# Kernel optimization log

Measured on AMD Instinct MI355X. Metric: run time of the kernel, lower is better.

The kernel has to match this reference:

```python
import jax, jax.numpy as jnp
import numpy as np

B, C, H, W = 8, 256, 96, 96
NQ, NCLS = 100, 12
OBJ_CH = NCLS - 2 + 1  # 11
EPS = 1e-6


def conv2d(x, w, b, pad):
    out = jax.lax.conv_general_dilated(x, w, (1, 1), [(pad, pad), (pad, pad)],
                                       dimension_numbers=('NCHW', 'OIHW', 'NCHW'))
    return out + b[None, :, None, None]


def conv1d(x, w, b):
    out = jax.lax.conv_general_dilated(x, w, (1,), [(0, 0)],
                                       dimension_numbers=('NCH', 'OIH', 'NCH'))
    return out + b[None, :, None]


def adaptive_avg_pool_1d(x, out_size):
    # x: [..., L]; torch AdaptiveAvgPool semantics: bin i = mean(x[floor(i*L/o):ceil((i+1)*L/o)])
    L = x.shape[-1]
    i = np.arange(out_size)
    starts = (i * L) // out_size
    ends = -((-(i + 1) * L) // out_size)
    csum = jnp.concatenate([jnp.zeros(x.shape[:-1] + (1,), x.dtype), jnp.cumsum(x, -1)], -1)
    sizes = jnp.asarray((ends - starts).astype(np.float32))
    return (csum[..., ends] - csum[..., starts]) / sizes


def local_max(p):
    # 8-neighbor local maximum with zero padding, thresholded at EPS
    pd = jnp.pad(p, ((0, 0), (0, 0), (1, 1), (1, 1)))
    m = ((p >= pd[:, :, :-2, 1:-1]) & (p >= pd[:, :, 2:, 1:-1]) &
         (p >= pd[:, :, 1:-1, :-2]) & (p >= pd[:, :, 1:-1, 2:]) &
         (p >= pd[:, :, :-2, :-2]) & (p >= pd[:, :, :-2, 2:]) &
         (p >= pd[:, :, 2:, :-2]) & (p >= pd[:, :, 2:, 2:]) & (p >= EPS))
    return m.astype(p.dtype)


def mask_and_nms(probs):
    # one-hot mask from argmax over foreground channels, then add local-max map
    oh = jax.nn.one_hot(jnp.argmax(probs[:, :-1], axis=1), probs.shape[1], axis=1, dtype=probs.dtype)
    p = probs * oh
    return p + local_max(p)


def head(x, w1, b1, w2, b2):
    return conv2d(jax.nn.relu(conv2d(x, w1, b1, 1)), w2, b2, 0)


def setup_inputs() -> dict:
    key = jax.random.key(0)
    ks = jax.random.split(key, 20)
    rn = lambda k, s: jax.random.normal(k, s, jnp.float32) * 0.02
    z = lambda n: jnp.zeros((n,), jnp.float32)
    return {
        'x': jax.random.normal(ks[0], (B, C, H, W), jnp.float32),
        'y': jax.random.normal(ks[1], (B, C, H, W), jnp.float32),
        'pos_embeddings': jax.random.normal(ks[2], (1, C, H, W), jnp.float32),
        'lw1': rn(ks[3], (C, C, 3, 3)), 'lb1': z(C),
        'lw2': rn(ks[4], (2, C, 1, 1)), 'lb2': z(2),
        'rw1': rn(ks[5], (C, C, 3, 3)), 'rb1': z(C),
        'rw2': rn(ks[6], (2, C, 1, 1)), 'rb2': z(2),
        'ow1': rn(ks[7], (C, C, 3, 3)), 'ob1': z(C),
        'ow2': rn(ks[8], (OBJ_CH, C, 1, 1)), 'ob2': z(OBJ_CH),
        'cw1': rn(ks[9], (64, C, 3, 3)), 'cb1': z(64),
        'cw2': rn(ks[10], (32, 64, 3, 3)), 'cb2': z(32),
        'cm_lw': rn(ks[11], (778 * 2, 778 * 32)), 'cm_lb': z(778 * 2),
        'c1d_w': rn(ks[12], (C, 2, 3)), 'c1d_b': z(C),
        'q_lw': rn(ks[13], (NQ * C, C)), 'q_lb': z(NQ * C),
    }


def reference(x, y, pos_embeddings, lw1, lb1, lw2, lb2, rw1, rb1, rw2, rb2,
              ow1, ob1, ow2, ob2, cw1, cb1, cw2, cb2, cm_lw, cm_lb,
              c1d_w, c1d_b, q_lw, q_lb):
    b = x.shape[0]
    left_logits = head(x, lw1, lb1, lw2, lb2)
    right_logits = head(x, rw1, rb1, rw2, rb2)
    obj_logits = head(x, ow1, ob1, ow2, ob2)

    left_p = mask_and_nms(jax.nn.softmax(left_logits, axis=1))
    right_p = mask_and_nms(jax.nn.softmax(right_logits, axis=1))
    obj_p = mask_and_nms(jax.nn.softmax(obj_logits, axis=1))

    hw = H * W
    idx_l = jax.lax.top_k(left_p[:, 0].reshape(b, hw), 40)[1]
    idx_r = jax.lax.top_k(right_p[:, 0].reshape(b, hw), 40)[1]
    idx_o = jax.lax.top_k(obj_p[:, :-1].reshape(b, OBJ_CH - 1, hw).max(axis=1), 20)[1]
    idx = jnp.concatenate([idx_l, idx_r, idx_o], axis=1)  # [B, 100]

    xf = x.reshape(b, C, hw)
    topk_proposals = jnp.take_along_axis(xf, jnp.broadcast_to(idx[:, None, :], (b, C, NQ)), axis=2)
    pf = jnp.broadcast_to(pos_embeddings, (b, C, H, W)).reshape(b, C, hw)
    topk_pos = jnp.take_along_axis(pf, jnp.broadcast_to(idx[:, None, :], (b, C, NQ)), axis=2)

    # contact map estimation branch
    h = jax.nn.relu(conv2d(y, cw1, cb1, 1))
    h = jax.nn.relu(conv2d(h, cw2, cb2, 1))  # [B,32,H,W]
    h = jnp.mean(h, axis=3)                  # adaptive pool width -> 1
    h = adaptive_avg_pool_1d(h, 778)         # [B,32,778]
    cm = h.reshape(b, -1) @ cm_lw.T + cm_lb  # [B,1556]
    contact_map = cm.reshape(b, 2, 778, 1)

    # ContactMapConvolution
    cc = conv1d(contact_map.reshape(b, 2, 778), c1d_w, c1d_b)  # [B,C,776]
    cc = jnp.mean(cc, axis=2)                                  # [B,C]
    feat = (cc @ q_lw.T + q_lb).reshape(b, C, NQ)              # [B,C,100]

    topk_proposals = topk_proposals + feat
    return (topk_proposals, topk_pos, left_logits, right_logits, obj_logits, contact_map)
```

## Files before the change

kernel.cpp:

```cpp
#include <hip/hip_runtime.h>
#include <float.h>
#include <math.h>

#define B_ 8
#define C_ 256
#define H_ 96
#define W_ 96
#define HW_ 9216
#define NQ_ 100
#define EPS_ 1e-6f
#define PADW_ 98
#define PADIMG_ 9604
#define PALLOC_ 76880

typedef unsigned short ushort_t;
typedef __attribute__((ext_vector_type(8))) short bf16x8;
typedef __attribute__((ext_vector_type(16))) float f32x16;

typedef __attribute__((address_space(3))) unsigned int as3_u32;
typedef __attribute__((address_space(1))) unsigned int as1_u32;

__device__ __forceinline__ void gl16(const void* g, void* l) {
    __builtin_amdgcn_global_load_lds(
        (const as1_u32*)(unsigned long long)g,
        (as3_u32*)(unsigned int)(unsigned long long)l, 16, 0, 0);
}

__device__ __forceinline__ ushort_t bf16_of(float v) {
    unsigned u = __float_as_uint(v);
    u += 0x7fffu + ((u >> 16) & 1u);
    return (ushort_t)(u >> 16);
}
__device__ __forceinline__ float f_of_bf16(ushort_t h) {
    return __uint_as_float((unsigned)h << 16);
}

__global__ __launch_bounds__(256)
void zero_border_kernel(ushort_t* __restrict__ bh, ushort_t* __restrict__ bl, int Cch)
{
    int per = 388 * Cch / 8;
    int id = blockIdx.x * 256 + threadIdx.x;
    if (id >= 8 * per) return;
    int b = id / per, i = id - b * per;
    int pi = (i * 8) / Cch, c8 = (i * 8) % Cch;
    int yy, xx;
    if (pi < 98)      { yy = 0;            xx = pi; }
    else if (pi < 196){ yy = 97;           xx = pi - 98; }
    else if (pi < 292){ yy = pi - 195;     xx = 0; }
    else              { yy = pi - 291;     xx = 97; }
    size_t base = ((size_t)b * PADIMG_ + yy * PADW_ + xx) * Cch + c8;
    *(bf16x8*)&bh[base] = (bf16x8)(short)0;
    *(bf16x8*)&bl[base] = (bf16x8)(short)0;
}

__global__ __launch_bounds__(256)
void tsplit_kernel(const float* __restrict__ in, ushort_t* __restrict__ oh,
                   ushort_t* __restrict__ ol, int Cch)
{
    __shared__ float T[32][33];
    const int tx = threadIdx.x & 31, ty = threadIdx.x >> 5;
    const int p0 = blockIdx.x * 32, ci0 = blockIdx.y * 32, b = blockIdx.z;
#pragma unroll
    for (int i = 0; i < 4; ++i)
        T[ty + 8*i][tx] = in[((size_t)b*Cch + ci0 + ty + 8*i)*HW_ + p0 + tx];
    __syncthreads();
    const int y = p0 / 96, x0 = p0 - y * 96;
    const size_t Pp = (size_t)b*PADIMG_ + (size_t)(y + 1)*PADW_ + x0 + 1;
#pragma unroll
    for (int i = 0; i < 4; ++i) {
        float v = T[tx][ty + 8*i];
        ushort_t hi = bf16_of(v);
        float lo = v - f_of_bf16(hi);
        size_t o = (Pp + ty + 8*i)*Cch + ci0 + tx;
        oh[o] = hi;
        ol[o] = bf16_of(lo);
    }
}

__global__ __launch_bounds__(256)
void repack_kernel(const float* __restrict__ w, ushort_t* __restrict__ wh,
                   ushort_t* __restrict__ wl, int Cout, int Cin)
{
    int id = blockIdx.x*256 + threadIdx.x;
    int tot = 9*Cout*Cin;
    if (id >= tot) return;
    int tap = id / (Cout*Cin);
    int r   = id - tap*(Cout*Cin);
    int g   = r / (Cout*16);
    int r2  = r - g*(Cout*16);
    int oc  = r2 >> 4, cr = r2 & 15;
    int ci  = g*16 + cr;
    float v = w[((size_t)oc*Cin + ci)*9 + tap];
    ushort_t hi = bf16_of(v);
    wh[id] = hi;
    wl[id] = bf16_of(v - f_of_bf16(hi));
}

__global__ __launch_bounds__(256)
void pack_heads3_kernel(const float* lb1, const float* rb1, const float* ob1,
                        const float* lw2, const float* rw2, const float* ow2,
                        const float* lb2, const float* rb2, const float* ob2,
                        float* __restrict__ bias1all, float* __restrict__ w2all,
                        float* __restrict__ b2all)
{
    int i = blockIdx.x * 256 + threadIdx.x;
    if (i < 768) bias1all[i] = (i < 256) ? lb1[i] : (i < 512) ? rb1[i-256] : ob1[i-512];
    if (i < 33) {
        int h = i / 11, k = i - h*11;
        b2all[i] = (h == 0) ? (k < 2 ? lb2[k] : 0.f)
                 : (h == 1) ? (k < 2 ? rb2[k] : 0.f)
                 : ob2[k];
    }
    if (i < 3*11*256) {
        int h = i / 2816, r = i - h*2816;
        int k = r / 256, oc = r - k*256;
        float v = 0.f;
        if (h == 0)      { if (k < 2) v = lw2[k*256 + oc]; }
        else if (h == 1) { if (k < 2) v = rw2[k*256 + oc]; }
        else             v = ow2[k*256 + oc];
        w2all[i] = v;
    }
}

template<int WM, int WN, int MFR, int NFR, int CIN, int MODE>
__global__ __launch_bounds__(WM*WN*64, (WM*WN + 3) / 4)
void conv_gemm_kernel(const ushort_t* __restrict__ Agh, const ushort_t* __restrict__ Agl,
                      const ushort_t* __restrict__ Wgh, const ushort_t* __restrict__ Wgl,
                      const float* __restrict__ bias1,
                      ushort_t* __restrict__ Oth, ushort_t* __restrict__ Otl,
                      float* __restrict__ outf)
{
    constexpr int NW    = WM*WN;
    constexpr int NT    = NW*64;
    constexpr int BM    = WM*MFR*32;
    constexpr int COUT  = WN*NFR*32;
    constexpr int NG    = CIN/16;
    constexpr int APAD  = 512;
    constexpr int ASZ   = 2*APAD*16;
    constexpr int AROUNDS = 32;
    static_assert(BM == 288, "BM must be 288");

    __shared__ __align__(16) ushort_t ALds[2*ASZ];

    const int tid  = threadIdx.x;
    const int lane = tid & 63;
    const int wid  = __builtin_amdgcn_readfirstlane(tid >> 6);
    const int wm   = wid / WN, wn = wid % WN;
    const int l31  = lane & 31, hh2 = lane >> 5;
    const int wnb  = wn * NFR * 32;

    const int cpx = gridDim.x >> 3;
    const int bid = (blockIdx.x & 7)*cpx + (blockIdx.x >> 3);
    const int bidx = bid >> 5;
    const int br   = bid & 31;
    const size_t S = (size_t)bidx*PADIMG_ + (size_t)(3*br)*PADW_;

    auto stageA = [&](int g, int sel) {
        ushort_t* dst = ALds + sel*ASZ;
#pragma unroll 1
        for (int c = wid; c < AROUNDS; c += NW) {
            int id = c*64 + lane;
            int split = id >> 10;
            int r2 = id & 1023;
            int row = r2 >> 1, slot = r2 & 1;
            int ch = slot ^ ((row >> 2) & 1);
            const ushort_t* src = (split ? Agl : Agh) + (S + row)*CIN + g*16 + ch*8;
            gl16(src, dst + (size_t)c*512);
        }
    };

    f32x16 acc[MFR][NFR];
#pragma unroll
    for (int i = 0; i < MFR; ++i)
#pragma unroll
        for (int j = 0; j < NFR; ++j)
#pragma unroll
            for (int r = 0; r < 16; ++r) acc[i][j][r] = 0.f;

    bf16x8 bh0[NFR], bl0[NFR], bh1[NFR], bl1[NFR], bh2[NFR], bl2[NFR];

#define LOADB(G, T, BH, BL)                                                    \
    {                                                                          \
        _Pragma("unroll")                                                      \
        for (int nf = 0; nf < NFR; ++nf) {                                     \
            size_t o = ((size_t)((T)*NG + (G))*COUT + (wnb + nf*32 + l31))*16  \
                       + hh2*8;                                                \
            BH[nf] = *(const bf16x8*)&Wgh[o];                                  \
            BL[nf] = *(const bf16x8*)&Wgl[o];                                  \
        }                                                                      \
    }

    stageA(0, 0);
    LOADB(0, 0, bh0, bl0);
    LOADB(0, 1, bh1, bl1);
    __builtin_amdgcn_sched_barrier(0);
    asm volatile("s_waitcnt vmcnt(%0)" :: "n"(4*NFR) : "memory");
    __builtin_amdgcn_s_barrier();
    __builtin_amdgcn_sched_barrier(0);

#define TAPBODY(T, BHC, BLC, BHN, BLN)                                         \
    {                                                                          \
        if ((T) <= 6)            LOADB(g,     (T)+2, BHN, BLN)                 \
        else if (g + 1 < NG)     LOADB(g+1,   (T)-7, BHN, BLN)                 \
        const int tapoff = ((T)/3)*PADW_ + ((T) % 3);                          \
        _Pragma("unroll")                                                      \
        for (int mf = 0; mf < MFR; ++mf) {                                     \
            int row = wm*PADW_ + tapoff + mf*32 + l31;                         \
            int o = abase + row*16 + ((hh2 ^ ((row >> 2) & 1)) << 3);          \
            bf16x8 ah = *(const bf16x8*)&ALds[o];                              \
            bf16x8 al = *(const bf16x8*)&ALds[o + APAD*16];                    \
            _Pragma("unroll")                                                  \
            for (int nf = 0; nf < NFR; ++nf) {                                 \
                acc[mf][nf] = __builtin_amdgcn_mfma_f32_32x32x16_bf16(         \
                    ah, BHC[nf], acc[mf][nf], 0, 0, 0);                        \
                acc[mf][nf] = __builtin_amdgcn_mfma_f32_32x32x16_bf16(         \
                    al, BHC[nf], acc[mf][nf], 0, 0, 0);                        \
                acc[mf][nf] = __builtin_amdgcn_mfma_f32_32x32x16_bf16(         \
                    ah, BLC[nf], acc[mf][nf], 0, 0, 0);                        \
            }                                                                  \
        }                                                                      \
    }

#pragma unroll 1
    for (int g = 0; g < NG; ++g) {
        if (g + 1 < NG) stageA(g + 1, (g + 1) & 1);
        const int abase = (g & 1) * ASZ;
        TAPBODY(0, bh0, bl0, bh2, bl2);
        TAPBODY(1, bh1, bl1, bh0, bl0);
        TAPBODY(2, bh2, bl2, bh1, bl1);
        TAPBODY(3, bh0, bl0, bh2, bl2);
        TAPBODY(4, bh1, bl1, bh0, bl0);
        TAPBODY(5, bh2, bl2, bh1, bl1);
        TAPBODY(6, bh0, bl0, bh2, bl2);
        TAPBODY(7, bh1, bl1, bh0, bl0);
        TAPBODY(8, bh2, bl2, bh1, bl1);
        __builtin_amdgcn_sched_barrier(0);
        asm volatile("s_waitcnt lgkmcnt(0)" ::: "memory");
        asm volatile("s_waitcnt vmcnt(%0)" :: "n"(4*NFR) : "memory");
        __builtin_amdgcn_s_barrier();
        __builtin_amdgcn_sched_barrier(0);
    }
#undef TAPBODY
#undef LOADB
    __syncthreads();

    float biasv[NFR];
#pragma unroll
    for (int nf = 0; nf < NFR; ++nf) biasv[nf] = bias1[wnb + nf*32 + l31];

    if constexpr (MODE == 1) {
#pragma unroll
        for (int mf = 0; mf < MFR; ++mf)
#pragma unroll
            for (int nf = 0; nf < NFR; ++nf)
#pragma unroll
                for (int r = 0; r < 16; ++r) {
                    float rr = fmaxf(acc[mf][nf][r] + biasv[nf], 0.f);
                    ushort_t hi = bf16_of(rr);
                    float lo = rr - f_of_bf16(hi);
                    int crow = (r & 3) + 8*(r >> 2) + 4*hh2;
                    int xx = mf*32 + crow;
                    size_t Pp = (size_t)bidx*PADIMG_
                              + (size_t)(3*br + wm + 1)*PADW_ + xx + 1;
                    size_t o = Pp*COUT + wnb + nf*32 + l31;
                    Oth[o] = hi;
                    Otl[o] = bf16_of(lo);
                }
    } else {
        float (*T)[BM + 1] = (float(*)[BM + 1])ALds;
#pragma unroll
        for (int mf = 0; mf < MFR; ++mf)
#pragma unroll
            for (int r = 0; r < 16; ++r) {
                float rr = fmaxf(acc[mf][0][r] + biasv[0], 0.f);
                int crow = (r & 3) + 8*(r >> 2) + 4*hh2;
                T[l31][wm*96 + mf*32 + crow] = rr;
            }
        __syncthreads();
        for (int i = tid; i < COUT*BM; i += NT) {
            int c = i / BM, m = i - c*BM;
            outf[((size_t)bidx*COUT + c)*HW_ + br*288 + m] = T[c][m];
        }
    }
}

template<int KK, int NH>
__global__ __launch_bounds__(256, 3)
void conv_sbt_kernel(const ushort_t* __restrict__ Agh, const ushort_t* __restrict__ Agl,
                     const ushort_t* __restrict__ w0h, const ushort_t* __restrict__ w0l,
                     const ushort_t* __restrict__ w1h, const ushort_t* __restrict__ w1l,
                     const float* __restrict__ bias1base, const float* __restrict__ w2base,
                     const float* __restrict__ b2base, float* __restrict__ dstbase)
{
    constexpr int NG = 16, APAD = 304, ASZ = 2*APAD*16, AGR = 19, MFR = 3, NFR = 2;
    __shared__ __align__(16) ushort_t ALds[2*ASZ];

    const int tid  = threadIdx.x;
    const int lane = tid & 63;
    const int wid  = __builtin_amdgcn_readfirstlane(tid >> 6);
    const int l31  = lane & 31, hh2 = lane >> 5;
    const int wnb  = wid * 64;

    const int h    = (NH == 1) ? 0 : (blockIdx.x / 768);
    const int subx = blockIdx.x - h*768;
    const int sub  = (subx & 7)*96 + (subx >> 3);
    const int bidx = sub / 96, prow = sub - bidx*96;
    const int pimg0 = prow * 96;
    const size_t S = (size_t)bidx*PADIMG_ + (size_t)prow*PADW_;

    const ushort_t* Wh = (h == 0) ? w0h : w1h;
    const ushort_t* Wl = (h == 0) ? w0l : w1l;
    const float* bias1 = bias1base + h*256;
    const float* w2    = w2base + (size_t)h*2816;
    const float* b2    = b2base + h*11;
    float* dst = dstbase + (size_t)h*147456;

    auto stageA = [&](int g, int sel) {
        ushort_t* dstl = ALds + sel*ASZ;
#pragma unroll 1
        for (int c = wid; c < AGR; c += 4) {
            int id = c*64 + lane;
            int split = id / (2*APAD);
            int r2 = id % (2*APAD);
            int row = r2 >> 1, slot = r2 & 1;
            int ch = slot ^ ((row >> 2) & 1);
            const ushort_t* src = (split ? Agl : Agh) + (S + row)*C_ + g*16 + ch*8;
            gl16(src, dstl + (size_t)c*512);
        }
    };

    f32x16 acc[MFR][NFR];
#pragma unroll
    for (int i = 0; i < MFR; ++i)
#pragma unroll
        for (int j = 0; j < NFR; ++j)
#pragma unroll
            for (int r = 0; r < 16; ++r) acc[i][j][r] = 0.f;

    bf16x8 bhX[NFR], blX[NFR], bhY[NFR], blY[NFR];

#define LOADB(G, T, BH, BL)                                                    \
    {                                                                          \
        _Pragma("unroll")                                                      \
        for (int nf = 0; nf < NFR; ++nf) {                                     \
            size_t o = ((size_t)((T)*NG + (G))*256 + (wnb + nf*32 + l31))*16   \
                       + hh2*8;                                                \
            BH[nf] = *(const bf16x8*)&Wh[o];                                   \
            BL[nf] = *(const bf16x8*)&Wl[o];                                   \
        }                                                                      \
    }

#define TAPBODY(G, T, ABASE, BHC, BLC, BHN, BLN)                               \
    {                                                                          \
        if ((T) < 8)             LOADB((G), (T)+1, BHN, BLN)                   \
        else if ((G) + 1 < NG)   LOADB((G)+1, 0, BHN, BLN)                     \
        const int tapoff = ((T)/3)*PADW_ + ((T) % 3);                          \
        _Pragma("unroll")                                                      \
        for (int mf = 0; mf < MFR; ++mf) {                                     \
            int row = tapoff + mf*32 + l31;                                    \
            int o = (ABASE) + row*16 + ((hh2 ^ ((row >> 2) & 1)) << 3);        \
            bf16x8 ah = *(const bf16x8*)&ALds[o];                              \
            bf16x8 al = *(const bf16x8*)&ALds[o + APAD*16];                    \
            _Pragma("unroll")                                                  \
            for (int nf = 0; nf < NFR; ++nf) {                                 \
                acc[mf][nf] = __builtin_amdgcn_mfma_f32_32x32x16_bf16(         \
                    ah, BHC[nf], acc[mf][nf], 0, 0, 0);                        \
                acc[mf][nf] = __builtin_amdgcn_mfma_f32_32x32x16_bf16(         \
                    al, BHC[nf], acc[mf][nf], 0, 0, 0);                        \
                acc[mf][nf] = __builtin_amdgcn_mfma_f32_32x32x16_bf16(         \
                    ah, BLC[nf], acc[mf][nf], 0, 0, 0);                        \
            }                                                                  \
        }                                                                      \
    }

#define GROUPBODY(G, ABASE, S0h, S0l, S1h, S1l)                                \
    {                                                                          \
        TAPBODY((G), 0, (ABASE), S0h, S0l, S1h, S1l);                          \
        TAPBODY((G), 1, (ABASE), S1h, S1l, S0h, S0l);                          \
        TAPBODY((G), 2, (ABASE), S0h, S0l, S1h, S1l);                          \
        TAPBODY((G), 3, (ABASE), S1h, S1l, S0h, S0l);                          \
        TAPBODY((G), 4, (ABASE), S0h, S0l, S1h, S1l);                          \
        TAPBODY((G), 5, (ABASE), S1h, S1l, S0h, S0l);                          \
        TAPBODY((G), 6, (ABASE), S0h, S0l, S1h, S1l);                          \
        TAPBODY((G), 7, (ABASE), S1h, S1l, S0h, S0l);                          \
        TAPBODY((G), 8, (ABASE), S0h, S0l, S1h, S1l);                          \
    }

#define GROUPEND                                                               \
    __builtin_amdgcn_sched_barrier(0);                                         \
    asm volatile("s_waitcnt lgkmcnt(0)" ::: "memory");                         \
    asm volatile("s_waitcnt vmcnt(%0)" :: "n"(2*NFR) : "memory");              \
    __builtin_amdgcn_s_barrier();                                              \
    __builtin_amdgcn_sched_barrier(0);

    stageA(0, 0);
    LOADB(0, 0, bhX, blX);
    __builtin_amdgcn_sched_barrier(0);
    asm volatile("s_waitcnt vmcnt(%0)" :: "n"(2*NFR) : "memory");
    __builtin_amdgcn_s_barrier();
    __builtin_amdgcn_sched_barrier(0);

#pragma unroll 1
    for (int g = 0; g < NG; g += 2) {
        if (g + 1 < NG) stageA(g + 1, 1);
        GROUPBODY(g, 0, bhX, blX, bhY, blY);
        GROUPEND
        if (g + 2 < NG) stageA(g + 2, 0);
        GROUPBODY(g + 1, ASZ, bhY, blY, bhX, blX);
        GROUPEND
    }
#undef GROUPEND
#undef GROUPBODY
#undef TAPBODY
#undef LOADB
    __syncthreads();

    float biasv[NFR];
#pragma unroll
    for (int nf = 0; nf < NFR; ++nf) biasv[nf] = bias1[wnb + nf*32 + l31];
    float w2v[NFR][KK];
#pragma unroll
    for (int nf = 0; nf < NFR; ++nf)
#pragma unroll
        for (int k = 0; k < KK; ++k) w2v[nf][k] = w2[k*256 + wnb + nf*32 + l31];

    float* Lacc = (float*)ALds;
#pragma unroll
    for (int mf = 0; mf < MFR; ++mf) {
#pragma unroll
        for (int r = 0; r < 16; ++r) {
            float v[KK];
#pragma unroll
            for (int k = 0; k < KK; ++k) v[k] = 0.f;
#pragma unroll
            for (int nf = 0; nf < NFR; ++nf) {
                float rr = fmaxf(acc[mf][nf][r] + biasv[nf], 0.f);
#pragma unroll
                for (int k = 0; k < KK; ++k) v[k] += rr * w2v[nf][k];
            }
#pragma unroll
            for (int k = 0; k < KK; ++k) {
                v[k] += __shfl_xor(v[k], 1);
                v[k] += __shfl_xor(v[k], 2);
                v[k] += __shfl_xor(v[k], 4);
                v[k] += __shfl_xor(v[k], 8);
                v[k] += __shfl_xor(v[k], 16);
            }
            if (l31 == 0) {
                int crow = (r & 3) + 8*(r >> 2) + 4*hh2;
                int row96 = mf*32 + crow;
#pragma unroll
                for (int k = 0; k < KK; ++k)
                    Lacc[((size_t)wid*96 + row96)*KK + k] = v[k];
            }
        }
    }
    __syncthreads();
    for (int i = tid; i < 96*KK; i += 256) {
        int row96 = i / KK, k = i - row96*KK;
        float s = b2[k];
#pragma unroll
        for (int w = 0; w < 4; ++w) s += Lacc[((size_t)w*96 + row96)*KK + k];
        dst[((size_t)bidx*KK + k)*HW_ + pimg0 + row96] = s;
    }
}

__global__ __launch_bounds__(256)
void prob2b_kernel(const float* __restrict__ l2, const float* __restrict__ l3,
                   float* __restrict__ pL, float* __restrict__ pR)
{
    const float* logits = blockIdx.y ? l3 : l2;
    float* p0 = blockIdx.y ? pR : pL;
    int i = blockIdx.x * 256 + threadIdx.x;
    if (i >= B_ * HW_) return;
    int b = i / HW_, pix = i - b * HW_;
    float l0 = logits[(size_t)b * 2 * HW_ + pix];
    float l1 = logits[(size_t)b * 2 * HW_ + HW_ + pix];
    float m = fmaxf(l0, l1);
    float e0 = expf(l0 - m), e1 = expf(l1 - m);
    p0[i] = e0 / (e0 + e1);
}

__global__ __launch_bounds__(256)
void score2b_kernel(const float* __restrict__ pL, const float* __restrict__ pR,
                    float* __restrict__ sL, float* __restrict__ sR)
{
    const float* p = blockIdx.y ? pR : pL;
    float* sc = blockIdx.y ? sR : sL;
    int i = blockIdx.x * 256 + threadIdx.x;
    if (i >= B_ * HW_) return;
    int pix = i % HW_;
    int yy = pix / W_, xx = pix - (pix / W_) * W_;
    float c = p[i];
    bool ok = (c >= EPS_);
    const float* pb = p + (i - pix);
#pragma unroll
    for (int dy = -1; dy <= 1; ++dy)
#pragma unroll
        for (int dx = -1; dx <= 1; ++dx) {
            if (dy == 0 && dx == 0) continue;
            int ny = yy + dy, nx = xx + dx;
            float v = 0.f;
            if (ny >= 0 && ny < H_ && nx >= 0 && nx < W_) v = pb[ny * W_ + nx];
            ok = ok && (c >= v);
        }
    sc[i] = c + (ok ? 1.f : 0.f);
}

__global__ __launch_bounds__(256)
void probobj_kernel(const float* __restrict__ logits, float* __restrict__ pval,
                    int* __restrict__ cstar)
{
    int i = blockIdx.x * 256 + threadIdx.x;
    if (i >= B_ * HW_) return;
    int b = i / HW_, pix = i - b * HW_;
    const float* lb = logits + (size_t)b * 11 * HW_ + pix;
    float l[11];
#pragma unroll
    for (int c2 = 0; c2 < 11; ++c2) l[c2] = lb[(size_t)c2 * HW_];
    float m = l[0];
#pragma unroll
    for (int c2 = 1; c2 < 11; ++c2) m = fmaxf(m, l[c2]);
    float sum = 0.f;
#pragma unroll
    for (int c2 = 0; c2 < 11; ++c2) sum += expf(l[c2] - m);
    int a = 0; float bestl = l[0];
#pragma unroll
    for (int c2 = 1; c2 < 10; ++c2)
        if (l[c2] > bestl) { bestl = l[c2]; a = c2; }
    pval[i] = expf(bestl - m) / sum;
    cstar[i] = a;
}

__global__ __launch_bounds__(256)
void score11_kernel(const float* __restrict__ p, const int* __restrict__ cs,
                    float* __restrict__ sc)
{
    int i = blockIdx.x * 256 + threadIdx.x;
    if (i >= B_ * HW_) return;
    int pix = i % HW_;
    int yy = pix / W_, xx = pix - (pix / W_) * W_;
    float c = p[i];
    int cc = cs[i];
    bool ok = (c >= EPS_);
    int base = i - pix;
#pragma unroll
    for (int dy = -1; dy <= 1; ++dy)
#pragma unroll
        for (int dx = -1; dx <= 1; ++dx) {
            if (dy == 0 && dx == 0) continue;
            int ny = yy + dy, nx = xx + dx;
            float v = 0.f;
            if (ny >= 0 && ny < H_ && nx >= 0 && nx < W_) {
                int n = base + ny * W_ + nx;
                v = (cs[n] == cc) ? p[n] : 0.f;
            }
            ok = ok && (c >= v);
        }
    sc[i] = c + (ok ? 1.f : 0.f);
}

__global__ __launch_bounds__(256)
void topk_kernel(const float* __restrict__ scL, const float* __restrict__ scR,
                 const float* __restrict__ scO, int* __restrict__ idx)
{
    __shared__ float sv[HW_];
    __shared__ float rv[256];
    __shared__ int   ri[256];
    const int h = blockIdx.x, b = blockIdx.y;
    const float* src = (h == 0) ? scL : (h == 1) ? scR : scO;
    const int k = (h == 2) ? 20 : 40;
    const int off = b * NQ_ + ((h == 0) ? 0 : (h == 1) ? 40 : 80);

    for (int t = threadIdx.x; t < HW_; t += 256) sv[t] = src[(size_t)b * HW_ + t];
    __syncthreads();

    for (int kk = 0; kk < k; ++kk) {
        float bestv = -FLT_MAX; int besti = HW_;
        for (int t = threadIdx.x; t < HW_; t += 256) {
            float v = sv[t];
            if (v > bestv) { bestv = v; besti = t; }
        }
        rv[threadIdx.x] = bestv; ri[threadIdx.x] = besti;
        __syncthreads();
        for (int s = 128; s > 0; s >>= 1) {
            if (threadIdx.x < s) {
                float v2 = rv[threadIdx.x + s]; int i2 = ri[threadIdx.x + s];
                if (v2 > rv[threadIdx.x] ||
                    (v2 == rv[threadIdx.x] && i2 < ri[threadIdx.x])) {
                    rv[threadIdx.x] = v2; ri[threadIdx.x] = i2;
                }
            }
            __syncthreads();
        }
        if (threadIdx.x == 0) { idx[off + kk] = ri[0]; sv[ri[0]] = -FLT_MAX; }
        __syncthreads();
    }
}

__global__ __launch_bounds__(128)
void pool_kernel(const float* __restrict__ h2, float* __restrict__ pooled)
{
    int bc = blockIdx.x;
    __shared__ float row[96];
    for (int hh = threadIdx.x; hh < 96; hh += 128) {
        const float* p = h2 + (size_t)bc * HW_ + hh * W_;
        float s = 0.f;
        for (int ww = 0; ww < 96; ++ww) s += p[ww];
        row[hh] = s * (1.f / 96.f);
    }
    __syncthreads();
    for (int i = threadIdx.x; i < 778; i += 128) {
        int s0 = (i * 96) / 778;
        int e0 = ((i + 1) * 96 + 777) / 778;
        float s = 0.f;
        for (int t = s0; t < e0; ++t) s += row[t];
        pooled[(size_t)bc * 778 + i] = s / (float)(e0 - s0);
    }
}

__global__ __launch_bounds__(256)
void cm_kernel(const float* __restrict__ pooled, const float* __restrict__ cm_lw,
               const float* __restrict__ cm_lb, float* __restrict__ out5)
{
    const int j = blockIdx.x;
    const float* wr = cm_lw + (size_t)j * 24896;
    float acc[8];
#pragma unroll
    for (int b = 0; b < 8; ++b) acc[b] = 0.f;
    for (int t = threadIdx.x; t < 24896; t += 256) {
        float w = wr[t];
#pragma unroll
        for (int b = 0; b < 8; ++b) acc[b] += w * pooled[(size_t)b * 24896 + t];
    }
    __shared__ float red[8][256];
#pragma unroll
    for (int b = 0; b < 8; ++b) red[b][threadIdx.x] = acc[b];
    __syncthreads();
    for (int s = 128; s > 0; s >>= 1) {
        if (threadIdx.x < s) {
#pragma unroll
            for (int b = 0; b < 8; ++b) red[b][threadIdx.x] += red[b][threadIdx.x + s];
        }
        __syncthreads();
    }
    if (threadIdx.x < 8)
        out5[(size_t)threadIdx.x * 1556 + j] = red[threadIdx.x][0] + cm_lb[j];
}

__global__ __launch_bounds__(256)
void c1d_kernel(const float* __restrict__ cmap, const float* __restrict__ w,
                const float* __restrict__ bias, float* __restrict__ ccmean)
{
    int b = blockIdx.x;
    __shared__ float r[2][778];
    __shared__ float T[2][3];
    for (int t = threadIdx.x; t < 1556; t += 256)
        r[t / 778][t % 778] = cmap[(size_t)b * 1556 + t];
    __syncthreads();
    if (threadIdx.x < 2) {
        int ic = threadIdx.x;
        float s = 0.f;
        for (int i2 = 0; i2 < 778; ++i2) s += r[ic][i2];
        T[ic][0] = s - r[ic][776] - r[ic][777];
        T[ic][1] = s - r[ic][0]   - r[ic][777];
        T[ic][2] = s - r[ic][0]   - r[ic][1];
    }
    __syncthreads();
    int oc = threadIdx.x;
    float a = 0.f;
#pragma unroll
    for (int ic = 0; ic < 2; ++ic)
#pragma unroll
        for (int k = 0; k < 3; ++k)
            a += w[oc * 6 + ic * 3 + k] * T[ic][k];
    ccmean[b * 256 + oc] = a / 776.f + bias[oc];
}

__global__ __launch_bounds__(256)
void feat_kernel(const float* __restrict__ ccmean, const float* __restrict__ q_lw,
                 const float* __restrict__ q_lb, float* __restrict__ feat)
{
    __shared__ float cc[8][256];
    for (int t = threadIdx.x; t < 2048; t += 256) cc[t >> 8][t & 255] = ccmean[t];
    __syncthreads();
    int j = blockIdx.x * 256 + threadIdx.x;
    const float* wr = q_lw + (size_t)j * 256;
    float acc[8];
#pragma unroll
    for (int b = 0; b < 8; ++b) acc[b] = 0.f;
    for (int c = 0; c < 256; ++c) {
        float wv = wr[c];
#pragma unroll
        for (int b = 0; b < 8; ++b) acc[b] += wv * cc[b][c];
    }
    float qb = q_lb[j];
#pragma unroll
    for (int b = 0; b < 8; ++b) feat[(size_t)b * 25600 + j] = acc[b] + qb;
}

__global__ __launch_bounds__(256)
void gather_kernel(const float* __restrict__ x, const float* __restrict__ pos,
                   const float* __restrict__ feat, const int* __restrict__ idx,
                   float* __restrict__ out0, float* __restrict__ out1)
{
    int t = blockIdx.x * 256 + threadIdx.x;
    if (t >= B_ * C_ * NQ_) return;
    int q = t % NQ_;
    int c2 = (t / NQ_) % C_;
    int b = t / (C_ * NQ_);
    int p = idx[b * NQ_ + q];
    out0[t] = x[((size_t)b * C_ + c2) * HW_ + p] + feat[(size_t)b * 25600 + c2 * NQ_ + q];
    out1[t] = pos[(size_t)c2 * HW_ + p];
}

extern "C" void kernel_launch(void* const* d_in, const int* in_sizes, int n_in,
                              void* d_out, int out_size, void* d_ws, size_t ws_size,
                              hipStream_t stream) {
    const float* x    = (const float*)d_in[0];
    const float* y    = (const float*)d_in[1];
    const float* pos  = (const float*)d_in[2];
    const float* lw1  = (const float*)d_in[3];  const float* lb1 = (const float*)d_in[4];
    const float* lw2  = (const float*)d_in[5];  const float* lb2 = (const float*)d_in[6];
    const float* rw1  = (const float*)d_in[7];  const float* rb1 = (const float*)d_in[8];
    const float* rw2  = (const float*)d_in[9];  const float* rb2 = (const float*)d_in[10];
    const float* ow1  = (const float*)d_in[11]; const float* ob1 = (const float*)d_in[12];
    const float* ow2  = (const float*)d_in[13]; const float* ob2 = (const float*)d_in[14];
    const float* cw1  = (const float*)d_in[15]; const float* cb1 = (const float*)d_in[16];
    const float* cw2  = (const float*)d_in[17]; const float* cb2 = (const float*)d_in[18];
    const float* cmlw = (const float*)d_in[19]; const float* cmlb = (const float*)d_in[20];
    const float* c1dw = (const float*)d_in[21]; const float* c1db = (const float*)d_in[22];
    const float* qlw  = (const float*)d_in[23]; const float* qlb  = (const float*)d_in[24];

    float* out  = (float*)d_out;
    float* out0 = out;
    float* out1 = out + 204800;
    float* out2 = out + 409600;
    float* out3 = out + 557056;
    float* out4 = out + 704512;
    float* out5 = out + 1515520;

    float* ws = (float*)d_ws;
    ushort_t* Rh   = (ushort_t*)(ws);
    ushort_t* Rl   = (ushort_t*)(ws + 9840640);
    ushort_t* h1h  = (ushort_t*)(ws + 19681280);
    ushort_t* h1l  = (ushort_t*)(ws + 22141440);
    float*    h2   = ws + 24601600;
    ushort_t* wLh  = (ushort_t*)(ws + 26960896);
    ushort_t* wLl  = (ushort_t*)(ws + 27255808);
    ushort_t* wRh  = (ushort_t*)(ws + 27550720);
    ushort_t* wRl  = (ushort_t*)(ws + 27845632);
    ushort_t* wOh  = (ushort_t*)(ws + 28140544);
    ushort_t* wOl  = (ushort_t*)(ws + 28435456);
    ushort_t* wc1h = (ushort_t*)(ws + 28730368);
    ushort_t* wc1l = (ushort_t*)(ws + 28804096);
    ushort_t* wc2h = (ushort_t*)(ws + 28877824);
    ushort_t* wc2l = (ushort_t*)(ws + 28887040);
    float* pooled  = ws + 28896256;
    float* ccmean  = ws + 29095424;
    float* feat    = ws + 29097472;
    float* pmapL   = ws + 29302272;
    int*   csmap   = (int*)(ws + 29376000);
    float* scL     = ws + 29449728;
    float* scR     = ws + 29523456;
    float* scO     = ws + 29597184;
    int*   idxb    = (int*)(ws + 29670912);
    float* bias1all= ws + 29671712;
    float* w2all   = ws + 29672480;
    float* b2all   = ws + 29680928;
    float* pmapR   = ws + 29680976;
    float* pmapO   = ws + 29754704;
    (void)in_sizes; (void)n_in; (void)out_size; (void)ws_size; (void)pos;

    zero_border_kernel<<<388, 256, 0, stream>>>(Rh, Rl, 256);
    zero_border_kernel<<<97,  256, 0, stream>>>(h1h, h1l, 64);
    repack_kernel<<<(9*256*256+255)/256, 256, 0, stream>>>(lw1, wLh, wLl, 256, 256);
    repack_kernel<<<(9*256*256+255)/256, 256, 0, stream>>>(rw1, wRh, wRl, 256, 256);
    repack_kernel<<<(9*256*256+255)/256, 256, 0, stream>>>(ow1, wOh, wOl, 256, 256);
    repack_kernel<<<(9*64*256+255)/256,  256, 0, stream>>>(cw1, wc1h, wc1l, 64, 256);
    repack_kernel<<<(9*32*64+255)/256,   256, 0, stream>>>(cw2, wc2h, wc2l, 32, 64);
    pack_heads3_kernel<<<33, 256, 0, stream>>>(lb1, rb1, ob1, lw2, rw2, ow2,
                                               lb2, rb2, ob2, bias1all, w2all, b2all);

    tsplit_kernel<<<dim3(288, 8, 8), 256, 0, stream>>>(y, Rh, Rl, 256);
    conv_gemm_kernel<3,2,3,1,256,1><<<256, 384, 0, stream>>>(
        Rh, Rl, wc1h, wc1l, cb1, h1h, h1l, nullptr);
    conv_gemm_kernel<3,1,3,1,64,2><<<256, 192, 0, stream>>>(
        h1h, h1l, wc2h, wc2l, cb2, nullptr, nullptr, h2);
    pool_kernel<<<256, 128, 0, stream>>>(h2, pooled);
    cm_kernel<<<1556, 256, 0, stream>>>(pooled, cmlw, cmlb, out5);
    c1d_kernel<<<8, 256, 0, stream>>>(out5, c1dw, c1db, ccmean);
    feat_kernel<<<100, 256, 0, stream>>>(ccmean, qlw, qlb, feat);

    tsplit_kernel<<<dim3(288, 8, 8), 256, 0, stream>>>(x, Rh, Rl, 256);
    conv_sbt_kernel<2,2><<<1536, 256, 0, stream>>>(
        Rh, Rl, wLh, wLl, wRh, wRl, bias1all, w2all, b2all, out2);
    conv_sbt_kernel<11,1><<<768, 256, 0, stream>>>(
        Rh, Rl, wOh, wOl, wOh, wOl, bias1all + 512, w2all + 2*2816,
        b2all + 22, out4);

    prob2b_kernel<<<dim3(288, 2), 256, 0, stream>>>(out2, out3, pmapL, pmapR);
    score2b_kernel<<<dim3(288, 2), 256, 0, stream>>>(pmapL, pmapR, scL, scR);
    probobj_kernel<<<288, 256, 0, stream>>>(out4, pmapO, csmap);
    score11_kernel<<<288, 256, 0, stream>>>(pmapO, csmap, scO);

    topk_kernel<<<dim3(3, 8), 256, 0, stream>>>(scL, scR, scO, idxb);
    gather_kernel<<<800, 256, 0, stream>>>(x, pos, feat, idxb, out0, out1);
}
```

Baseline: 1.146 ms.

## Merge small launches and rewrite top-k with cached per-thread packed-key maxima

Several small kernels are combined through a grid y dimension: zero-border twice, head weight repack three times, and the prob and score kernels into one each. The top-k kernel now keeps a per-thread best key that packs the score bits with the index, reduces it with wave shuffles plus a four-entry shared merge, and rescans only in the thread that owned the selected element. This replaces a full LDS scan and a tree reduction with many barriers on each of up to 40 iterations. Ordering on raw float bits is only valid for non-negative scores, which probabilities plus a 0/1 flag satisfy, and ties still go to the lower index.

```diff
diff --git a/kernel.cpp b/kernel.cpp
--- a/kernel.cpp
+++ b/kernel.cpp
@@ -35,11 +35,9 @@
     return __uint_as_float((unsigned)h << 16);
 }
 
-__global__ __launch_bounds__(256)
-void zero_border_kernel(ushort_t* __restrict__ bh, ushort_t* __restrict__ bl, int Cch)
+__device__ __forceinline__ void zb_body(ushort_t* bh, ushort_t* bl, int Cch, int id)
 {
     int per = 388 * Cch / 8;
-    int id = blockIdx.x * 256 + threadIdx.x;
     if (id >= 8 * per) return;
     int b = id / per, i = id - b * per;
     int pi = (i * 8) / Cch, c8 = (i * 8) % Cch;
@@ -54,6 +52,15 @@
 }
 
 __global__ __launch_bounds__(256)
+void zero_border2_kernel(ushort_t* __restrict__ bh0, ushort_t* __restrict__ bl0,
+                         ushort_t* __restrict__ bh1, ushort_t* __restrict__ bl1)
+{
+    int id = blockIdx.x * 256 + threadIdx.x;
+    if (blockIdx.y == 0) zb_body(bh0, bl0, 256, id);
+    else                 zb_body(bh1, bl1, 64, id);
+}
+
+__global__ __launch_bounds__(256)
 void tsplit_kernel(const float* __restrict__ in, ushort_t* __restrict__ oh,
                    ushort_t* __restrict__ ol, int Cch)
 {
@@ -77,11 +84,9 @@
     }
 }
 
-__global__ __launch_bounds__(256)
-void repack_kernel(const float* __restrict__ w, ushort_t* __restrict__ wh,
-                   ushort_t* __restrict__ wl, int Cout, int Cin)
-{
-    int id = blockIdx.x*256 + threadIdx.x;
+__device__ __forceinline__ void repack_body(const float* w, ushort_t* wh,
+                                            ushort_t* wl, int Cout, int Cin, int id)
+{
     int tot = 9*Cout*Cin;
     if (id >= tot) return;
     int tap = id / (Cout*Cin);
@@ -94,6 +99,26 @@
     ushort_t hi = bf16_of(v);
     wh[id] = hi;
     wl[id] = bf16_of(v - f_of_bf16(hi));
+}
+
+__global__ __launch_bounds__(256)
+void repack_kernel(const float* __restrict__ w, ushort_t* __restrict__ wh,
+                   ushort_t* __restrict__ wl, int Cout, int Cin)
+{
+    repack_body(w, wh, wl, Cout, Cin, blockIdx.x*256 + threadIdx.x);
+}
+
+__global__ __launch_bounds__(256)
+void repack3_kernel(const float* __restrict__ wL, const float* __restrict__ wR,
+                    const float* __restrict__ wO,
+                    ushort_t* __restrict__ wLh, ushort_t* __restrict__ wLl,
+                    ushort_t* __restrict__ wRh, ushort_t* __restrict__ wRl,
+                    ushort_t* __restrict__ wOh, ushort_t* __restrict__ wOl)
+{
+    int id = blockIdx.x*256 + threadIdx.x;
+    if (blockIdx.y == 0)      repack_body(wL, wLh, wLl, 256, 256, id);
+    else if (blockIdx.y == 1) repack_body(wR, wRh, wRl, 256, 256, id);
+    else                      repack_body(wO, wOh, wOl, 256, 256, id);
 }
 
 __global__ __launch_bounds__(256)
@@ -466,97 +491,84 @@
 }
 
 __global__ __launch_bounds__(256)
-void prob2b_kernel(const float* __restrict__ l2, const float* __restrict__ l3,
-                   float* __restrict__ pL, float* __restrict__ pR)
-{
-    const float* logits = blockIdx.y ? l3 : l2;
-    float* p0 = blockIdx.y ? pR : pL;
+void prob3_kernel(const float* __restrict__ l2, const float* __restrict__ l3,
+                  const float* __restrict__ l4, float* __restrict__ pL,
+                  float* __restrict__ pR, float* __restrict__ pO,
+                  int* __restrict__ cstar)
+{
     int i = blockIdx.x * 256 + threadIdx.x;
     if (i >= B_ * HW_) return;
     int b = i / HW_, pix = i - b * HW_;
-    float l0 = logits[(size_t)b * 2 * HW_ + pix];
-    float l1 = logits[(size_t)b * 2 * HW_ + HW_ + pix];
-    float m = fmaxf(l0, l1);
-    float e0 = expf(l0 - m), e1 = expf(l1 - m);
-    p0[i] = e0 / (e0 + e1);
-}
-
-__global__ __launch_bounds__(256)
-void score2b_kernel(const float* __restrict__ pL, const float* __restrict__ pR,
-                    float* __restrict__ sL, float* __restrict__ sR)
-{
-    const float* p = blockIdx.y ? pR : pL;
-    float* sc = blockIdx.y ? sR : sL;
+    if (blockIdx.y < 2) {
+        const float* logits = blockIdx.y ? l3 : l2;
+        float* p0 = blockIdx.y ? pR : pL;
+        float v0 = logits[(size_t)b * 2 * HW_ + pix];
+        float v1 = logits[(size_t)b * 2 * HW_ + HW_ + pix];
+        float m = fmaxf(v0, v1);
+        float e0 = expf(v0 - m), e1 = expf(v1 - m);
+        p0[i] = e0 / (e0 + e1);
+    } else {
+        const float* lb = l4 + (size_t)b * 11 * HW_ + pix;
+        float l[11];
+#pragma unroll
+        for (int c2 = 0; c2 < 11; ++c2) l[c2] = lb[(size_t)c2 * HW_];
+        float m = l[0];
+#pragma unroll
+        for (int c2 = 1; c2 < 11; ++c2) m = fmaxf(m, l[c2]);
+        float sum = 0.f;
+#pragma unroll
+        for (int c2 = 0; c2 < 11; ++c2) sum += expf(l[c2] - m);
+        int a = 0; float bestl = l[0];
+#pragma unroll
+        for (int c2 = 1; c2 < 10; ++c2)
+            if (l[c2] > bestl) { bestl = l[c2]; a = c2; }
+        pO[i] = expf(bestl - m) / sum;
+        cstar[i] = a;
+    }
+}
+
+__global__ __launch_bounds__(256)
+void score3_kernel(const float* __restrict__ pL, const float* __restrict__ pR,
+                   const float* __restrict__ pO, const int* __restrict__ cs,
+                   float* __restrict__ sL, float* __restrict__ sR,
+                   float* __restrict__ sO)
+{
     int i = blockIdx.x * 256 + threadIdx.x;
     if (i >= B_ * HW_) return;
     int pix = i % HW_;
     int yy = pix / W_, xx = pix - (pix / W_) * W_;
+    const float* p = (blockIdx.y == 0) ? pL : (blockIdx.y == 1) ? pR : pO;
+    float* sc = (blockIdx.y == 0) ? sL : (blockIdx.y == 1) ? sR : sO;
     float c = p[i];
     bool ok = (c >= EPS_);
-    const float* pb = p + (i - pix);
-#pragma unroll
-    for (int dy = -1; dy <= 1; ++dy)
-#pragma unroll
-        for (int dx = -1; dx <= 1; ++dx) {
-            if (dy == 0 && dx == 0) continue;
-            int ny = yy + dy, nx = xx + dx;
-            float v = 0.f;
-            if (ny >= 0 && ny < H_ && nx >= 0 && nx < W_) v = pb[ny * W_ + nx];
-            ok = ok && (c >= v);
-        }
-    sc[i] = c + (ok ? 1.f : 0.f);
-}
-
-__global__ __launch_bounds__(256)
-void probobj_kernel(const float* __restrict__ logits, float* __restrict__ pval,
-                    int* __restrict__ cstar)
-{
-    int i = blockIdx.x * 256 + threadIdx.x;
-    if (i >= B_ * HW_) return;
-    int b = i / HW_, pix = i - b * HW_;
-    const float* lb = logits + (size_t)b * 11 * HW_ + pix;
-    float l[11];
-#pragma unroll
-    for (int c2 = 0; c2 < 11; ++c2) l[c2] = lb[(size_t)c2 * HW_];
-    float m = l[0];
-#pragma unroll
-    for (int c2 = 1; c2 < 11; ++c2) m = fmaxf(m, l[c2]);
-    float sum = 0.f;
-#pragma unroll
-    for (int c2 = 0; c2 < 11; ++c2) sum += expf(l[c2] - m);
-    int a = 0; float bestl = l[0];
-#pragma unroll
-    for (int c2 = 1; c2 < 10; ++c2)
-        if (l[c2] > bestl) { bestl = l[c2]; a = c2; }
-    pval[i] = expf(bestl - m) / sum;
-    cstar[i] = a;
-}
-
-__global__ __launch_bounds__(256)
-void score11_kernel(const float* __restrict__ p, const int* __restrict__ cs,
-                    float* __restrict__ sc)
-{
-    int i = blockIdx.x * 256 + threadIdx.x;
-    if (i >= B_ * HW_) return;
-    int pix = i % HW_;
-    int yy = pix / W_, xx = pix - (pix / W_) * W_;
-    float c = p[i];
-    int cc = cs[i];
-    bool ok = (c >= EPS_);
     int base = i - pix;
-#pragma unroll
-    for (int dy = -1; dy <= 1; ++dy)
-#pragma unroll
-        for (int dx = -1; dx <= 1; ++dx) {
-            if (dy == 0 && dx == 0) continue;
-            int ny = yy + dy, nx = xx + dx;
-            float v = 0.f;
-            if (ny >= 0 && ny < H_ && nx >= 0 && nx < W_) {
-                int n = base + ny * W_ + nx;
-                v = (cs[n] == cc) ? p[n] : 0.f;
+    if (blockIdx.y < 2) {
+#pragma unroll
+        for (int dy = -1; dy <= 1; ++dy)
+#pragma unroll
+            for (int dx = -1; dx <= 1; ++dx) {
+                if (dy == 0 && dx == 0) continue;
+                int ny = yy + dy, nx = xx + dx;
+                float v = 0.f;
+                if (ny >= 0 && ny < H_ && nx >= 0 && nx < W_) v = p[base + ny * W_ + nx];
+                ok = ok && (c >= v);
             }
-            ok = ok && (c >= v);
-        }
+    } else {
+        int cc = cs[i];
+#pragma unroll
+        for (int dy = -1; dy <= 1; ++dy)
+#pragma unroll
+            for (int dx = -1; dx <= 1; ++dx) {
+                if (dy == 0 && dx == 0) continue;
+                int ny = yy + dy, nx = xx + dx;
+                float v = 0.f;
+                if (ny >= 0 && ny < H_ && nx >= 0 && nx < W_) {
+                    int n = base + ny * W_ + nx;
+                    v = (cs[n] == cc) ? p[n] : 0.f;
+                }
+                ok = ok && (c >= v);
+            }
+    }
     sc[i] = c + (ok ? 1.f : 0.f);
 }
 
@@ -565,36 +577,54 @@
                  const float* __restrict__ scO, int* __restrict__ idx)
 {
     __shared__ float sv[HW_];
-    __shared__ float rv[256];
-    __shared__ int   ri[256];
+    __shared__ unsigned long long wb[4];
+    __shared__ int bsh;
     const int h = blockIdx.x, b = blockIdx.y;
     const float* src = (h == 0) ? scL : (h == 1) ? scR : scO;
     const int k = (h == 2) ? 20 : 40;
     const int off = b * NQ_ + ((h == 0) ? 0 : (h == 1) ? 40 : 80);
-
-    for (int t = threadIdx.x; t < HW_; t += 256) sv[t] = src[(size_t)b * HW_ + t];
-    __syncthreads();
+    const int tid = threadIdx.x, lane = tid & 63, wid = tid >> 6;
+
+    for (int t = tid; t < HW_; t += 256) sv[t] = src[(size_t)b * HW_ + t];
+    __syncthreads();
+
+    unsigned long long best = 0;
+    for (int t = tid; t < HW_; t += 256) {
+        float v = sv[t];
+        unsigned long long key = ((unsigned long long)__float_as_uint(v) << 32)
+                               | (unsigned)(HW_ - t);
+        if (v >= 0.f && key > best) best = key;
+    }
 
     for (int kk = 0; kk < k; ++kk) {
-        float bestv = -FLT_MAX; int besti = HW_;
-        for (int t = threadIdx.x; t < HW_; t += 256) {
-            float v = sv[t];
-            if (v > bestv) { bestv = v; besti = t; }
+        unsigned long long r = best;
+#pragma unroll
+        for (int o = 32; o > 0; o >>= 1) {
+            unsigned long long q = __shfl_xor(r, o);
+            if (q > r) r = q;
         }
-        rv[threadIdx.x] = bestv; ri[threadIdx.x] = besti;
+        if (lane == 0) wb[wid] = r;
         __syncthreads();
-        for (int s = 128; s > 0; s >>= 1) {
-            if (threadIdx.x < s) {
-                float v2 = rv[threadIdx.x + s]; int i2 = ri[threadIdx.x + s];
-                if (v2 > rv[threadIdx.x] ||
-                    (v2 == rv[threadIdx.x] && i2 < ri[threadIdx.x])) {
-                    rv[threadIdx.x] = v2; ri[threadIdx.x] = i2;
-                }
+        if (tid == 0) {
+            unsigned long long m = wb[0];
+            if (wb[1] > m) m = wb[1];
+            if (wb[2] > m) m = wb[2];
+            if (wb[3] > m) m = wb[3];
+            int bi = HW_ - (int)(unsigned)(m & 0xffffffffu);
+            idx[off + kk] = bi;
+            sv[bi] = -1.f;
+            bsh = bi;
+        }
+        __syncthreads();
+        if ((bsh & 255) == tid) {
+            best = 0;
+            for (int t = tid; t < HW_; t += 256) {
+                float v = sv[t];
+                unsigned long long key = ((unsigned long long)__float_as_uint(v) << 32)
+                                       | (unsigned)(HW_ - t);
+                if (v >= 0.f && key > best) best = key;
             }
-            __syncthreads();
         }
-        if (threadIdx.x == 0) { idx[off + kk] = ri[0]; sv[ri[0]] = -FLT_MAX; }
-        __syncthreads();
     }
 }
 
@@ -772,11 +802,9 @@
     float* pmapO   = ws + 29754704;
     (void)in_sizes; (void)n_in; (void)out_size; (void)ws_size; (void)pos;
 
-    zero_border_kernel<<<388, 256, 0, stream>>>(Rh, Rl, 256);
-    zero_border_kernel<<<97,  256, 0, stream>>>(h1h, h1l, 64);
-    repack_kernel<<<(9*256*256+255)/256, 256, 0, stream>>>(lw1, wLh, wLl, 256, 256);
-    repack_kernel<<<(9*256*256+255)/256, 256, 0, stream>>>(rw1, wRh, wRl, 256, 256);
-    repack_kernel<<<(9*256*256+255)/256, 256, 0, stream>>>(ow1, wOh, wOl, 256, 256);
+    zero_border2_kernel<<<dim3(388, 2), 256, 0, stream>>>(Rh, Rl, h1h, h1l);
+    repack3_kernel<<<dim3((9*256*256+255)/256, 3), 256, 0, stream>>>(
+        lw1, rw1, ow1, wLh, wLl, wRh, wRl, wOh, wOl);
     repack_kernel<<<(9*64*256+255)/256,  256, 0, stream>>>(cw1, wc1h, wc1l, 64, 256);
     repack_kernel<<<(9*32*64+255)/256,   256, 0, stream>>>(cw2, wc2h, wc2l, 32, 64);
     pack_heads3_kernel<<<33, 256, 0, stream>>>(lb1, rb1, ob1, lw2, rw2, ow2,
@@ -799,10 +827,10 @@
         Rh, Rl, wOh, wOl, wOh, wOl, bias1all + 512, w2all + 2*2816,
         b2all + 22, out4);
 
-    prob2b_kernel<<<dim3(288, 2), 256, 0, stream>>>(out2, out3, pmapL, pmapR);
-    score2b_kernel<<<dim3(288, 2), 256, 0, stream>>>(pmapL, pmapR, scL, scR);
-    probobj_kernel<<<288, 256, 0, stream>>>(out4, pmapO, csmap);
-    score11_kernel<<<288, 256, 0, stream>>>(pmapO, csmap, scO);
+    prob3_kernel<<<dim3(288, 3), 256, 0, stream>>>(out2, out3, out4,
+                                                   pmapL, pmapR, pmapO, csmap);
+    score3_kernel<<<dim3(288, 3), 256, 0, stream>>>(pmapL, pmapR, pmapO, csmap,
+                                                    scL, scR, scO);
 
     topk_kernel<<<dim3(3, 8), 256, 0, stream>>>(scL, scR, scO, idxb);
     gather_kernel<<<800, 256, 0, stream>>>(x, pos, feat, idxb, out0, out1);
```

Measured after the change: 1.134 ms (median of 2 runs). About the same (-1.0%).
